# Optimization experiments

Hardware: AMD Instinct MI355X
Metric: run time of the kernel (lower is better)

Reference implementation:

```python
import jax, jax.numpy as jnp
import numpy as np

HIDDEN = 2048
N_HEADS = 16
N_KV_HEADS = 4
HEAD_DIM = HIDDEN // N_HEADS  # 128
N_GROUPS = N_HEADS // N_KV_HEADS  # 4
ROPE_THETA = 10000.0


def _rope_tables(dim, max_len, theta):
    freqs = 1.0 / theta ** (jnp.arange(0, dim, 2, dtype=jnp.float32) / dim)
    pos = jnp.arange(max_len, dtype=jnp.float32)
    ang = jnp.outer(pos, freqs)  # [T, dim//2]
    return jnp.cos(ang), jnp.sin(ang)


def _apply_rope(x, cos, sin):
    # x: [B, H, T, hd]; interleaved-pair rotation, matching torch stack+flatten
    c = cos[None, None]  # [1,1,T,hd//2]
    s = sin[None, None]
    x1, x2 = x[..., 0::2], x[..., 1::2]
    out = jnp.stack([x1 * c - x2 * s, x1 * s + x2 * c], axis=-1)
    return out.reshape(x.shape)


def setup_inputs() -> dict:
    key = jax.random.key(0)
    ks = jax.random.split(key, 5)
    B, T = 2, 2048
    sc = 0.02
    return {
        "x": jax.random.normal(ks[0], (B, T, HIDDEN), jnp.float32),
        "wq": jax.random.normal(ks[1], (HIDDEN, HIDDEN), jnp.float32) * sc,
        "wk": jax.random.normal(ks[2], (HIDDEN, N_KV_HEADS * HEAD_DIM), jnp.float32) * sc,
        "wv": jax.random.normal(ks[3], (HIDDEN, N_KV_HEADS * HEAD_DIM), jnp.float32) * sc,
        "wo": jax.random.normal(ks[4], (HIDDEN, HIDDEN), jnp.float32) * sc,
    }


def reference(x, wq, wk, wv, wo):
    B, T, D = x.shape
    cos, sin = _rope_tables(HEAD_DIM, T, ROPE_THETA)

    Q = (x @ wq).reshape(B, T, N_HEADS, HEAD_DIM).transpose(0, 2, 1, 3)      # [B,H,T,hd]
    K = (x @ wk).reshape(B, T, N_KV_HEADS, HEAD_DIM).transpose(0, 2, 1, 3)   # [B,Hk,T,hd]
    V = (x @ wv).reshape(B, T, N_KV_HEADS, HEAD_DIM).transpose(0, 2, 1, 3)

    Q = _apply_rope(Q, cos, sin)
    K = _apply_rope(K, cos, sin)

    # GQA: view Q as [B, Hk, G, T, hd] and contract against shared K/V heads
    Qg = Q.reshape(B, N_KV_HEADS, N_GROUPS, T, HEAD_DIM)
    scale = 1.0 / jnp.sqrt(jnp.asarray(HEAD_DIM, jnp.float32))
    scores = jnp.einsum('bkgqd,bkpd->bkgqp', Qg, K) * scale  # [B,Hk,G,T,T]

    causal = jnp.tril(jnp.ones((T, T), dtype=bool))
    scores = jnp.where(causal, scores, jnp.finfo(scores.dtype).min)
    probs = jax.nn.softmax(scores, axis=-1)

    out = jnp.einsum('bkgqp,bkpd->bkgqd', probs, V)           # [B,Hk,G,T,hd]
    out = out.reshape(B, N_HEADS, T, HEAD_DIM).transpose(0, 2, 1, 3).reshape(B, T, D)
    return out @ wo
```

## Files before the change

### kernel.cpp

```cpp
#include <hip/hip_runtime.h>
#include <stdint.h>


#define T_SEQ 2048
#define NHEAD 16
#define NKVH  4
#define HD    128
#define BT    4096

typedef unsigned short u16;
typedef __attribute__((ext_vector_type(8))) __bf16 bf16x8;
typedef __attribute__((ext_vector_type(8))) u16    u16x8;
typedef __attribute__((ext_vector_type(4))) u16    u16x4;
typedef __attribute__((ext_vector_type(4))) float  f32x4;

__device__ __forceinline__ u16 f2bf(float f) {
  uint32_t x = __float_as_uint(f);
  return (u16)((x + 0x7FFFu + ((x >> 16) & 1u)) >> 16);
}
__device__ __forceinline__ float bf2f(u16 u) {
  return __uint_as_float(((uint32_t)u) << 16);
}

__device__ __forceinline__ void gll16(const void* g, void* l) {
  __builtin_amdgcn_global_load_lds(
      (const __attribute__((address_space(1))) unsigned int*)g,
      (__attribute__((address_space(3))) unsigned int*)l, 16, 0, 0);
}

__global__ __launch_bounds__(256) void k_cast_x(const float* __restrict__ src,
                                                u16* __restrict__ dst) {
  size_t id = (size_t)blockIdx.x * 256 + threadIdx.x;
  f32x4 v = *reinterpret_cast<const f32x4*>(src + id * 4);
  u16x4 o;
  o[0] = f2bf(v[0]); o[1] = f2bf(v[1]); o[2] = f2bf(v[2]); o[3] = f2bf(v[3]);
  *reinterpret_cast<u16x4*>(dst + id * 4) = o;
}

__global__ __launch_bounds__(256) void k_transpose_cast(const float* __restrict__ src,
                                                        u16* __restrict__ dst,
                                                        int R, int C) {
  __shared__ float tile[32][33];
  int c0 = blockIdx.x * 32, r0 = blockIdx.y * 32;
  int tx = threadIdx.x & 31, ty = threadIdx.x >> 5;
#pragma unroll
  for (int i = 0; i < 4; ++i)
    tile[ty + i * 8][tx] = src[(size_t)(r0 + ty + i * 8) * C + c0 + tx];
  __syncthreads();
#pragma unroll
  for (int i = 0; i < 4; ++i)
    dst[(size_t)(c0 + ty + i * 8) * R + r0 + tx] = f2bf(tile[tx][ty + i * 8]);
}

__global__ __launch_bounds__(256) void k_transpose_v(const u16* __restrict__ src,
                                                     u16* __restrict__ dst) {
  __shared__ u16 tile[32][34];
  int slice = blockIdx.z;
  src += (size_t)slice * T_SEQ * HD;
  dst += (size_t)slice * HD * T_SEQ;
  int d0 = blockIdx.x * 32, t0 = blockIdx.y * 32;
  int tx = threadIdx.x & 31, ty = threadIdx.x >> 5;
#pragma unroll
  for (int i = 0; i < 4; ++i)
    tile[ty + i * 8][tx] = src[(size_t)(t0 + ty + i * 8) * HD + d0 + tx];
  __syncthreads();
#pragma unroll
  for (int i = 0; i < 4; ++i)
    dst[(size_t)(d0 + ty + i * 8) * T_SEQ + t0 + tx] = tile[tx][ty + i * 8];
}

__global__ __launch_bounds__(256) void k_rope_tables(float* __restrict__ tc,
                                                     float* __restrict__ ts) {
  int id = blockIdx.x * 256 + threadIdx.x;
  int pos = id >> 6, i = id & 63;
  float freq = exp2f(-(float)i * (13.287712379549449f / 64.0f));
  float ang = (float)pos * freq;
  tc[id] = cosf(ang);
  ts[id] = sinf(ang);
}

__global__ __launch_bounds__(256) void k_rope_apply(u16* __restrict__ buf,
                                                    const float* __restrict__ tc,
                                                    const float* __restrict__ ts,
                                                    float scale) {
  int id = blockIdx.x * 256 + threadIdx.x;
  int i8 = id & 15;
  int t  = (id >> 4) & (T_SEQ - 1);
  int bh = id >> 15;
  u16* p = buf + ((size_t)bh * T_SEQ + t) * HD + i8 * 8;
  u16x8 v = *reinterpret_cast<u16x8*>(p);
  f32x4 c = *reinterpret_cast<const f32x4*>(tc + t * 64 + i8 * 4);
  f32x4 s = *reinterpret_cast<const f32x4*>(ts + t * 64 + i8 * 4);
  u16x8 o;
#pragma unroll
  for (int j = 0; j < 4; ++j) {
    float x1 = bf2f(v[2 * j]), x2 = bf2f(v[2 * j + 1]);
    o[2 * j]     = f2bf((x1 * c[j] - x2 * s[j]) * scale);
    o[2 * j + 1] = f2bf((x1 * s[j] + x2 * c[j]) * scale);
  }
  *reinterpret_cast<u16x8*>(p) = o;
}

template <int EPI>
__global__ __launch_bounds__(256) void k_gemm(const u16* __restrict__ A,
                                              const u16* __restrict__ W0,
                                              const u16* __restrict__ W1,
                                              const u16* __restrict__ W2,
                                              u16* __restrict__ Qb,
                                              u16* __restrict__ Kb,
                                              u16* __restrict__ Vb,
                                              float* __restrict__ Cf) {
  __shared__ u16 As[128 * 32];
  __shared__ u16 Bs[128 * 32];
  int t = threadIdx.x;
  int bx = blockIdx.x, by = blockIdx.y;
  int ncol0 = bx * 128;
  const u16* Bt;
  if (EPI == 0) {
    if (ncol0 < 2048)      Bt = W0 + (size_t)ncol0 * 2048;
    else if (ncol0 < 2560) Bt = W1 + (size_t)(ncol0 - 2048) * 2048;
    else                   Bt = W2 + (size_t)(ncol0 - 2560) * 2048;
  } else {
    Bt = W0 + (size_t)ncol0 * 2048;
  }
  const u16* ga = A  + (size_t)(by * 128 + (t >> 2)) * 2048 + (t & 3) * 8;
  const u16* gb = Bt + (size_t)(t >> 2) * 2048 + (t & 3) * 8;
  int w = t >> 6, l = t & 63;
  int wr = w >> 1, wc = w & 1;
  int lr = l & 15, lh = l >> 4;
  f32x4 acc[4][4] = {};
  for (int kb = 0; kb < 2048; kb += 32) {
    __syncthreads();
    gll16(ga,             &As[t * 8]);
    gll16(ga + 64 * 2048, &As[2048 + t * 8]);
    gll16(gb,             &Bs[t * 8]);
    gll16(gb + 64 * 2048, &Bs[2048 + t * 8]);
    ga += 32; gb += 32;
    __syncthreads();
    bf16x8 af[4], bw[4];
#pragma unroll
    for (int fr = 0; fr < 4; ++fr)
      af[fr] = *reinterpret_cast<const bf16x8*>(&As[(wr * 64 + fr * 16 + lr) * 32 + lh * 8]);
#pragma unroll
    for (int fc = 0; fc < 4; ++fc)
      bw[fc] = *reinterpret_cast<const bf16x8*>(&Bs[(wc * 64 + fc * 16 + lr) * 32 + lh * 8]);
#pragma unroll
    for (int fr = 0; fr < 4; ++fr)
#pragma unroll
      for (int fc = 0; fc < 4; ++fc)
        acc[fr][fc] = __builtin_amdgcn_mfma_f32_16x16x32_bf16(af[fr], bw[fc], acc[fr][fc], 0, 0, 0);
  }
  int row0 = by * 128 + wr * 64;
  int col0 = ncol0 + wc * 64;
#pragma unroll
  for (int fr = 0; fr < 4; ++fr)
#pragma unroll
    for (int fc = 0; fc < 4; ++fc)
#pragma unroll
      for (int r = 0; r < 4; ++r) {
        int row = row0 + fr * 16 + lh * 4 + r;
        int col = col0 + fc * 16 + lr;
        float v = acc[fr][fc][r];
        if (EPI == 1) {
          Cf[(size_t)row * 2048 + col] = v;
        } else {
          int b = row >> 11, tt = row & 2047;
          if (col < 2048) {
            int h = col >> 7, d = col & 127;
            Qb[((size_t)(b * NHEAD + h) * T_SEQ + tt) * HD + d] = f2bf(v);
          } else if (col < 2560) {
            int c2 = col - 2048; int h = c2 >> 7, d = c2 & 127;
            Kb[((size_t)(b * NKVH + h) * T_SEQ + tt) * HD + d] = f2bf(v);
          } else {
            int c2 = col - 2560; int h = c2 >> 7, d = c2 & 127;
            Vb[((size_t)(b * NKVH + h) * T_SEQ + tt) * HD + d] = f2bf(v);
          }
        }
      }
}

__global__ __launch_bounds__(512, 4) void k_attn(const u16* __restrict__ Q,
                                                 const u16* __restrict__ K,
                                                 const u16* __restrict__ Vt,
                                                 u16* __restrict__ O) {
  __shared__ u16 KbS[2][64 * 128];
  __shared__ u16 VbS[128 * 64];
  __shared__ u16 Plds[8][16][72];

  int blk   = blockIdx.x;
  int slice = blk & 7;
  int half  = (blk >> 3) & 1;
  int g     = blk >> 4;
  int lvl   = (g < 16) ? g : 47 - g;
  int nt    = 32 - lvl;
  int w = threadIdx.x >> 6, l = threadIdx.x & 63;
  int lr = l & 15, lh = l >> 4;
  int hg = w & 3, q4 = half * 2 + (w >> 2);
  int qrow0 = ((nt - 1) * 4 + q4) * 16;
  int b = slice >> 2, kvh = slice & 3, h = kvh * 4 + hg;

  const u16* Qp = Q  + ((size_t)(b * NHEAD + h) * T_SEQ) * HD;
  const u16* Kp = K  + ((size_t)(b * NKVH + kvh) * T_SEQ) * HD;
  const u16* Vp = Vt + ((size_t)(b * NKVH + kvh) * HD) * T_SEQ;

  bf16x8 qf[4];
#pragma unroll
  for (int ks = 0; ks < 4; ++ks)
    qf[ks] = *reinterpret_cast<const bf16x8*>(Qp + (size_t)(qrow0 + lr) * HD + ks * 32 + lh * 8);

  f32x4 o[8] = {};
  float mrun[4], lrun[4];
#pragma unroll
  for (int r = 0; r < 4; ++r) { mrun[r] = -1e30f; lrun[r] = 0.f; }

  int kx = (lr & 7) << 4;

#pragma unroll
  for (int i = 0; i < 2; ++i) {
    int L = (w * 2 + i) * 1024 + l * 16;
    int P = L ^ (((L >> 8) & 7) << 4);
    gll16((const char*)Kp + P, (char*)KbS[0] + L);
  }
  __syncthreads();

  int cur = 0;
  for (int it = 0; it < nt; ++it) {
    int t0 = it * 64;
#pragma unroll
    for (int i = 0; i < 2; ++i) {
      int L = (w * 2 + i) * 1024 + l * 16;
      int P = L ^ (((L >> 7) & 7) << 4);
      int d = P >> 7, tb = P & 127;
      gll16((const char*)(Vp + t0) + (size_t)d * (T_SEQ * 2) + tb, (char*)VbS + L);
    }
    if (it + 1 < nt) {
#pragma unroll
      for (int i = 0; i < 2; ++i) {
        int L = (w * 2 + i) * 1024 + l * 16;
        int P = L ^ (((L >> 8) & 7) << 4);
        gll16((const char*)Kp + (size_t)(t0 + 64) * 256 + P, (char*)KbS[cur ^ 1] + L);
      }
    }
    const char* kb = (const char*)KbS[cur];
    f32x4 s[4] = {};
#pragma unroll
    for (int ct = 0; ct < 4; ++ct) {
      bf16x8 kf[4];
#pragma unroll
      for (int ks = 0; ks < 4; ++ks)
        kf[ks] = *reinterpret_cast<const bf16x8*>(
            kb + ct * 4096 + lr * 256 + ((ks * 64 + lh * 16) ^ kx));
#pragma unroll
      for (int ks = 0; ks < 4; ++ks)
        s[ct] = __builtin_amdgcn_mfma_f32_16x16x32_bf16(qf[ks], kf[ks], s[ct], 0, 0, 0);
    }
    if (it == nt - 1) {
#pragma unroll
      for (int ct = 0; ct < 4; ++ct) {
        int tcol = t0 + ct * 16 + lr;
#pragma unroll
        for (int r = 0; r < 4; ++r)
          if (tcol > qrow0 + lh * 4 + r) s[ct][r] = -1e30f;
      }
    }
#pragma unroll
    for (int r = 0; r < 4; ++r) {
      float rm = fmaxf(fmaxf(s[0][r], s[1][r]), fmaxf(s[2][r], s[3][r]));
      rm = fmaxf(rm, __shfl_xor(rm, 1));
      rm = fmaxf(rm, __shfl_xor(rm, 2));
      rm = fmaxf(rm, __shfl_xor(rm, 4));
      rm = fmaxf(rm, __shfl_xor(rm, 8));
      float nm = fmaxf(mrun[r], rm);
      float fs = __expf(mrun[r] - nm);
      float rowsum = 0.f;
#pragma unroll
      for (int ct = 0; ct < 4; ++ct) {
        float p = __expf(s[ct][r] - nm);
        s[ct][r] = p;
        rowsum += p;
      }
      rowsum += __shfl_xor(rowsum, 1);
      rowsum += __shfl_xor(rowsum, 2);
      rowsum += __shfl_xor(rowsum, 4);
      rowsum += __shfl_xor(rowsum, 8);
      lrun[r] = lrun[r] * fs + rowsum;
      mrun[r] = nm;
#pragma unroll
      for (int cd = 0; cd < 8; ++cd) o[cd][r] *= fs;
    }
#pragma unroll
    for (int ct = 0; ct < 4; ++ct)
#pragma unroll
      for (int r = 0; r < 4; ++r)
        Plds[w][lh * 4 + r][ct * 16 + lr] = f2bf(s[ct][r]);
    bf16x8 pf[2];
#pragma unroll
    for (int ks = 0; ks < 2; ++ks)
      pf[ks] = *reinterpret_cast<const bf16x8*>(&Plds[w][lr][ks * 32 + lh * 8]);

    __syncthreads();

    const char* vb = (const char*)VbS;
#pragma unroll
    for (int cd = 0; cd < 8; ++cd) {
      bf16x8 vf0 = *reinterpret_cast<const bf16x8*>(
          vb + cd * 2048 + lr * 128 + ((0 * 64 + lh * 16) ^ kx));
      bf16x8 vf1 = *reinterpret_cast<const bf16x8*>(
          vb + cd * 2048 + lr * 128 + ((1 * 64 + lh * 16) ^ kx));
      o[cd] = __builtin_amdgcn_mfma_f32_16x16x32_bf16(pf[0], vf0, o[cd], 0, 0, 0);
      o[cd] = __builtin_amdgcn_mfma_f32_16x16x32_bf16(pf[1], vf1, o[cd], 0, 0, 0);
    }
    __syncthreads();
    cur ^= 1;
  }
  float inv[4];
#pragma unroll
  for (int r = 0; r < 4; ++r) inv[r] = 1.0f / lrun[r];
#pragma unroll
  for (int cd = 0; cd < 8; ++cd)
#pragma unroll
    for (int r = 0; r < 4; ++r) {
      int row = qrow0 + lh * 4 + r;
      int col = h * HD + cd * 16 + lr;
      O[((size_t)(b * T_SEQ + row)) * 2048 + col] = f2bf(o[cd][r] * inv[r]);
    }
}

extern "C" void kernel_launch(void* const* d_in, const int* in_sizes, int n_in,
                              void* d_out, int out_size, void* d_ws, size_t ws_size,
                              hipStream_t stream) {
  const float* x  = (const float*)d_in[0];
  const float* wq = (const float*)d_in[1];
  const float* wk = (const float*)d_in[2];
  const float* wv = (const float*)d_in[3];
  const float* wo = (const float*)d_in[4];
  float* out = (float*)d_out;

  char* ws = (char*)d_ws;
  size_t off = 0;
  auto alloc = [&](size_t bytes) {
    char* p = ws + off;
    off = (off + bytes + 255) & ~(size_t)255;
    return p;
  };
  u16* xb   = (u16*)alloc((size_t)BT * 2048 * 2);
  u16* wqt  = (u16*)alloc((size_t)2048 * 2048 * 2);
  u16* wkt  = (u16*)alloc((size_t)512 * 2048 * 2);
  u16* wvt  = (u16*)alloc((size_t)512 * 2048 * 2);
  u16* wot  = (u16*)alloc((size_t)2048 * 2048 * 2);
  u16* Qb   = (u16*)alloc((size_t)BT * 2048 * 2);
  u16* Kb   = (u16*)alloc((size_t)2 * NKVH * T_SEQ * HD * 2);
  u16* Vb   = (u16*)alloc((size_t)2 * NKVH * T_SEQ * HD * 2);
  u16* Vtb  = (u16*)alloc((size_t)2 * NKVH * T_SEQ * HD * 2);
  float* tabc = (float*)alloc((size_t)T_SEQ * 64 * 4);
  float* tabs = (float*)alloc((size_t)T_SEQ * 64 * 4);
  u16* Ob = xb;
  (void)in_sizes; (void)n_in; (void)out_size; (void)ws_size;

  k_cast_x<<<dim3(8192), dim3(256), 0, stream>>>(x, xb);
  k_transpose_cast<<<dim3(64, 64), dim3(256), 0, stream>>>(wq, wqt, 2048, 2048);
  k_transpose_cast<<<dim3(16, 64), dim3(256), 0, stream>>>(wk, wkt, 2048, 512);
  k_transpose_cast<<<dim3(16, 64), dim3(256), 0, stream>>>(wv, wvt, 2048, 512);
  k_transpose_cast<<<dim3(64, 64), dim3(256), 0, stream>>>(wo, wot, 2048, 2048);
  k_rope_tables<<<dim3(512), dim3(256), 0, stream>>>(tabc, tabs);
  k_gemm<0><<<dim3(24, 32), dim3(256), 0, stream>>>(xb, wqt, wkt, wvt, Qb, Kb, Vb, nullptr);
  k_rope_apply<<<dim3(4096), dim3(256), 0, stream>>>(Qb, tabc, tabs, 0.08838834764831845f);
  k_rope_apply<<<dim3(1024), dim3(256), 0, stream>>>(Kb, tabc, tabs, 1.0f);
  k_transpose_v<<<dim3(4, 64, 8), dim3(256), 0, stream>>>(Vb, Vtb);
  k_attn<<<dim3(512), dim3(512), 0, stream>>>(Qb, Kb, Vtb, Ob);
  k_gemm<1><<<dim3(16, 32), dim3(256), 0, stream>>>(Ob, wot, nullptr, nullptr,
                                                    nullptr, nullptr, nullptr, out);
}
```

Before: 332.3 us.

## Merge prep and post kernels, defer softmax rescale, add MFMA priority hints

Collapses the cast, weight-transpose and rope-table kernels into one prep launch, and the two rope-apply kernels plus the V transpose into one post launch, to cut launch gaps. In attention, the output rescale is skipped when no row max grows anywhere in the wave. The per-row sum reduction across lanes is moved out of the loop to the final normalisation. s_setprio hints are also placed around the MFMA blocks. The merged kernels add branching per block, and the rescale skip adds a wave vote on every tile.

```diff
diff --git a/kernel.cpp b/kernel.cpp
--- a/kernel.cpp
+++ b/kernel.cpp
@@ -28,77 +28,96 @@
       (__attribute__((address_space(3))) unsigned int*)l, 16, 0, 0);
 }
 
-__global__ __launch_bounds__(256) void k_cast_x(const float* __restrict__ src,
-                                                u16* __restrict__ dst) {
-  size_t id = (size_t)blockIdx.x * 256 + threadIdx.x;
-  f32x4 v = *reinterpret_cast<const f32x4*>(src + id * 4);
-  u16x4 o;
-  o[0] = f2bf(v[0]); o[1] = f2bf(v[1]); o[2] = f2bf(v[2]); o[3] = f2bf(v[3]);
-  *reinterpret_cast<u16x4*>(dst + id * 4) = o;
-}
-
-__global__ __launch_bounds__(256) void k_transpose_cast(const float* __restrict__ src,
-                                                        u16* __restrict__ dst,
-                                                        int R, int C) {
+__global__ __launch_bounds__(256) void k_prep(const float* __restrict__ x,
+                                              const float* __restrict__ wq,
+                                              const float* __restrict__ wk,
+                                              const float* __restrict__ wv,
+                                              const float* __restrict__ wo,
+                                              u16* __restrict__ xb,
+                                              u16* __restrict__ wqt,
+                                              u16* __restrict__ wkt,
+                                              u16* __restrict__ wvt,
+                                              u16* __restrict__ wot,
+                                              float* __restrict__ tc,
+                                              float* __restrict__ ts) {
   __shared__ float tile[32][33];
-  int c0 = blockIdx.x * 32, r0 = blockIdx.y * 32;
-  int tx = threadIdx.x & 31, ty = threadIdx.x >> 5;
+  int blk = blockIdx.x, tid = threadIdx.x;
+  if (blk < 8192) {
+    size_t id = (size_t)blk * 256 + tid;
+    f32x4 v = *reinterpret_cast<const f32x4*>(x + id * 4);
+    u16x4 o;
+    o[0] = f2bf(v[0]); o[1] = f2bf(v[1]); o[2] = f2bf(v[2]); o[3] = f2bf(v[3]);
+    *reinterpret_cast<u16x4*>(xb + id * 4) = o;
+    return;
+  }
+  if (blk >= 18432) {
+    int id = (blk - 18432) * 256 + tid;
+    int pos = id >> 6, i = id & 63;
+    float freq = exp2f(-(float)i * (13.287712379549449f / 64.0f));
+    float ang = (float)pos * freq;
+    tc[id] = cosf(ang);
+    ts[id] = sinf(ang);
+    return;
+  }
+  const float* src; u16* dst; int C; int g;
+  if (blk < 12288)      { src = wq; dst = wqt; C = 2048; g = blk - 8192;
+  } else if (blk < 16384){ src = wo; dst = wot; C = 2048; g = blk - 12288;
+  } else if (blk < 17408){ src = wk; dst = wkt; C = 512;  g = blk - 16384;
+  } else                 { src = wv; dst = wvt; C = 512;  g = blk - 17408; }
+  int xt = (C == 2048) ? (g & 63) : (g & 15);
+  int yt = (C == 2048) ? (g >> 6) : (g >> 4);
+  int c0 = xt * 32, r0 = yt * 32;
+  int tx = tid & 31, ty = tid >> 5;
 #pragma unroll
   for (int i = 0; i < 4; ++i)
     tile[ty + i * 8][tx] = src[(size_t)(r0 + ty + i * 8) * C + c0 + tx];
   __syncthreads();
 #pragma unroll
   for (int i = 0; i < 4; ++i)
-    dst[(size_t)(c0 + ty + i * 8) * R + r0 + tx] = f2bf(tile[tx][ty + i * 8]);
-}
-
-__global__ __launch_bounds__(256) void k_transpose_v(const u16* __restrict__ src,
-                                                     u16* __restrict__ dst) {
-  __shared__ u16 tile[32][34];
-  int slice = blockIdx.z;
-  src += (size_t)slice * T_SEQ * HD;
-  dst += (size_t)slice * HD * T_SEQ;
-  int d0 = blockIdx.x * 32, t0 = blockIdx.y * 32;
-  int tx = threadIdx.x & 31, ty = threadIdx.x >> 5;
+    dst[(size_t)(c0 + ty + i * 8) * 2048 + r0 + tx] = f2bf(tile[tx][ty + i * 8]);
+}
+
+__global__ __launch_bounds__(256) void k_post(u16* __restrict__ Qb,
+                                              u16* __restrict__ Kb,
+                                              const u16* __restrict__ Vb,
+                                              u16* __restrict__ Vtb,
+                                              const float* __restrict__ tc,
+                                              const float* __restrict__ ts) {
+  __shared__ u16 vt[32][34];
+  int blk = blockIdx.x, tid = threadIdx.x;
+  if (blk < 5120) {
+    u16* buf; int id; float scale;
+    if (blk < 4096) { buf = Qb; id = blk * 256 + tid; scale = 0.08838834764831845f; }
+    else            { buf = Kb; id = (blk - 4096) * 256 + tid; scale = 1.0f; }
+    int i8 = id & 15;
+    int t  = (id >> 4) & (T_SEQ - 1);
+    int bh = id >> 15;
+    u16* p = buf + ((size_t)bh * T_SEQ + t) * HD + i8 * 8;
+    u16x8 v = *reinterpret_cast<u16x8*>(p);
+    f32x4 c = *reinterpret_cast<const f32x4*>(tc + t * 64 + i8 * 4);
+    f32x4 s = *reinterpret_cast<const f32x4*>(ts + t * 64 + i8 * 4);
+    u16x8 o;
+#pragma unroll
+    for (int j = 0; j < 4; ++j) {
+      float x1 = bf2f(v[2 * j]), x2 = bf2f(v[2 * j + 1]);
+      o[2 * j]     = f2bf((x1 * c[j] - x2 * s[j]) * scale);
+      o[2 * j + 1] = f2bf((x1 * s[j] + x2 * c[j]) * scale);
+    }
+    *reinterpret_cast<u16x8*>(p) = o;
+    return;
+  }
+  int g = blk - 5120;
+  int slice = g & 7, d0 = ((g >> 3) & 3) * 32, t0 = (g >> 5) * 32;
+  const u16* src = Vb + (size_t)slice * T_SEQ * HD;
+  u16* dst = Vtb + (size_t)slice * HD * T_SEQ;
+  int tx = tid & 31, ty = tid >> 5;
 #pragma unroll
   for (int i = 0; i < 4; ++i)
-    tile[ty + i * 8][tx] = src[(size_t)(t0 + ty + i * 8) * HD + d0 + tx];
+    vt[ty + i * 8][tx] = src[(size_t)(t0 + ty + i * 8) * HD + d0 + tx];
   __syncthreads();
 #pragma unroll
   for (int i = 0; i < 4; ++i)
-    dst[(size_t)(d0 + ty + i * 8) * T_SEQ + t0 + tx] = tile[tx][ty + i * 8];
-}
-
-__global__ __launch_bounds__(256) void k_rope_tables(float* __restrict__ tc,
-                                                     float* __restrict__ ts) {
-  int id = blockIdx.x * 256 + threadIdx.x;
-  int pos = id >> 6, i = id & 63;
-  float freq = exp2f(-(float)i * (13.287712379549449f / 64.0f));
-  float ang = (float)pos * freq;
-  tc[id] = cosf(ang);
-  ts[id] = sinf(ang);
-}
-
-__global__ __launch_bounds__(256) void k_rope_apply(u16* __restrict__ buf,
-                                                    const float* __restrict__ tc,
-                                                    const float* __restrict__ ts,
-                                                    float scale) {
-  int id = blockIdx.x * 256 + threadIdx.x;
-  int i8 = id & 15;
-  int t  = (id >> 4) & (T_SEQ - 1);
-  int bh = id >> 15;
-  u16* p = buf + ((size_t)bh * T_SEQ + t) * HD + i8 * 8;
-  u16x8 v = *reinterpret_cast<u16x8*>(p);
-  f32x4 c = *reinterpret_cast<const f32x4*>(tc + t * 64 + i8 * 4);
-  f32x4 s = *reinterpret_cast<const f32x4*>(ts + t * 64 + i8 * 4);
-  u16x8 o;
-#pragma unroll
-  for (int j = 0; j < 4; ++j) {
-    float x1 = bf2f(v[2 * j]), x2 = bf2f(v[2 * j + 1]);
-    o[2 * j]     = f2bf((x1 * c[j] - x2 * s[j]) * scale);
-    o[2 * j + 1] = f2bf((x1 * s[j] + x2 * c[j]) * scale);
-  }
-  *reinterpret_cast<u16x8*>(p) = o;
+    dst[(size_t)(d0 + ty + i * 8) * T_SEQ + t0 + tx] = vt[tx][ty + i * 8];
 }
 
 template <int EPI>
@@ -250,9 +269,11 @@
       for (int ks = 0; ks < 4; ++ks)
         kf[ks] = *reinterpret_cast<const bf16x8*>(
             kb + ct * 4096 + lr * 256 + ((ks * 64 + lh * 16) ^ kx));
+      __builtin_amdgcn_s_setprio(1);
 #pragma unroll
       for (int ks = 0; ks < 4; ++ks)
         s[ct] = __builtin_amdgcn_mfma_f32_16x16x32_bf16(qf[ks], kf[ks], s[ct], 0, 0, 0);
+      __builtin_amdgcn_s_setprio(0);
     }
     if (it == nt - 1) {
 #pragma unroll
@@ -263,6 +284,8 @@
           if (tcol > qrow0 + lh * 4 + r) s[ct][r] = -1e30f;
       }
     }
+    float fs[4], rsum[4];
+    bool grow = false;
 #pragma unroll
     for (int r = 0; r < 4; ++r) {
       float rm = fmaxf(fmaxf(s[0][r], s[1][r]), fmaxf(s[2][r], s[3][r]));
@@ -271,22 +294,28 @@
       rm = fmaxf(rm, __shfl_xor(rm, 4));
       rm = fmaxf(rm, __shfl_xor(rm, 8));
       float nm = fmaxf(mrun[r], rm);
-      float fs = __expf(mrun[r] - nm);
-      float rowsum = 0.f;
+      grow = grow || (nm > mrun[r]);
+      fs[r] = __expf(mrun[r] - nm);
+      mrun[r] = nm;
+      float rs = 0.f;
 #pragma unroll
       for (int ct = 0; ct < 4; ++ct) {
         float p = __expf(s[ct][r] - nm);
         s[ct][r] = p;
-        rowsum += p;
+        rs += p;
       }
-      rowsum += __shfl_xor(rowsum, 1);
-      rowsum += __shfl_xor(rowsum, 2);
-      rowsum += __shfl_xor(rowsum, 4);
-      rowsum += __shfl_xor(rowsum, 8);
-      lrun[r] = lrun[r] * fs + rowsum;
-      mrun[r] = nm;
-#pragma unroll
-      for (int cd = 0; cd < 8; ++cd) o[cd][r] *= fs;
+      rsum[r] = rs;
+    }
+    if (__any(grow)) {
+#pragma unroll
+      for (int r = 0; r < 4; ++r) {
+        lrun[r] = lrun[r] * fs[r] + rsum[r];
+#pragma unroll
+        for (int cd = 0; cd < 8; ++cd) o[cd][r] *= fs[r];
+      }
+    } else {
+#pragma unroll
+      for (int r = 0; r < 4; ++r) lrun[r] += rsum[r];
     }
 #pragma unroll
     for (int ct = 0; ct < 4; ++ct)
@@ -307,15 +336,24 @@
           vb + cd * 2048 + lr * 128 + ((0 * 64 + lh * 16) ^ kx));
       bf16x8 vf1 = *reinterpret_cast<const bf16x8*>(
           vb + cd * 2048 + lr * 128 + ((1 * 64 + lh * 16) ^ kx));
+      __builtin_amdgcn_s_setprio(1);
       o[cd] = __builtin_amdgcn_mfma_f32_16x16x32_bf16(pf[0], vf0, o[cd], 0, 0, 0);
       o[cd] = __builtin_amdgcn_mfma_f32_16x16x32_bf16(pf[1], vf1, o[cd], 0, 0, 0);
+      __builtin_amdgcn_s_setprio(0);
     }
     __syncthreads();
     cur ^= 1;
   }
   float inv[4];
 #pragma unroll
-  for (int r = 0; r < 4; ++r) inv[r] = 1.0f / lrun[r];
+  for (int r = 0; r < 4; ++r) {
+    float tsum = lrun[r];
+    tsum += __shfl_xor(tsum, 1);
+    tsum += __shfl_xor(tsum, 2);
+    tsum += __shfl_xor(tsum, 4);
+    tsum += __shfl_xor(tsum, 8);
+    inv[r] = 1.0f / tsum;
+  }
 #pragma unroll
   for (int cd = 0; cd < 8; ++cd)
 #pragma unroll
@@ -357,16 +395,11 @@
   u16* Ob = xb;
   (void)in_sizes; (void)n_in; (void)out_size; (void)ws_size;
 
-  k_cast_x<<<dim3(8192), dim3(256), 0, stream>>>(x, xb);
-  k_transpose_cast<<<dim3(64, 64), dim3(256), 0, stream>>>(wq, wqt, 2048, 2048);
-  k_transpose_cast<<<dim3(16, 64), dim3(256), 0, stream>>>(wk, wkt, 2048, 512);
-  k_transpose_cast<<<dim3(16, 64), dim3(256), 0, stream>>>(wv, wvt, 2048, 512);
-  k_transpose_cast<<<dim3(64, 64), dim3(256), 0, stream>>>(wo, wot, 2048, 2048);
-  k_rope_tables<<<dim3(512), dim3(256), 0, stream>>>(tabc, tabs);
+  k_prep<<<dim3(18944), dim3(256), 0, stream>>>(x, wq, wk, wv, wo,
+                                                xb, wqt, wkt, wvt, wot,
+                                                tabc, tabs);
   k_gemm<0><<<dim3(24, 32), dim3(256), 0, stream>>>(xb, wqt, wkt, wvt, Qb, Kb, Vb, nullptr);
-  k_rope_apply<<<dim3(4096), dim3(256), 0, stream>>>(Qb, tabc, tabs, 0.08838834764831845f);
-  k_rope_apply<<<dim3(1024), dim3(256), 0, stream>>>(Kb, tabc, tabs, 1.0f);
-  k_transpose_v<<<dim3(4, 64, 8), dim3(256), 0, stream>>>(Vb, Vtb);
+  k_post<<<dim3(7168), dim3(256), 0, stream>>>(Qb, Kb, Vb, Vtb, tabc, tabs);
   k_attn<<<dim3(512), dim3(512), 0, stream>>>(Qb, Kb, Vtb, Ob);
   k_gemm<1><<<dim3(16, 32), dim3(256), 0, stream>>>(Ob, wot, nullptr, nullptr,
                                                     nullptr, nullptr, nullptr, out);
```

After: 341.5 us. +2.8%, slower.
